# Kernel optimization log

Hardware: AMD Instinct MI355X
Metric: run time of the kernel (lower is better)

## Reference

```python
import jax, jax.numpy as jnp
import numpy as np

EPS = 1e-5

def layer_norm(x, g, b):
    mu = jnp.mean(x, axis=-1, keepdims=True)
    var = jnp.var(x, axis=-1, keepdims=True)
    return (x - mu) * jax.lax.rsqrt(var + EPS) * g + b

def mlp2_ln(x, w1, b1, g, bt, w2, b2):
    # 2-layer NN: Linear -> LayerNorm -> GELU -> Linear
    h = jax.nn.gelu(layer_norm(x @ w1 + b1, g, bt))
    return h @ w2 + b2

def mlp2(x, w1, b1, w2, b2):
    # 2-layer NN without norm: Linear -> GELU -> Linear
    return jax.nn.gelu(x @ w1 + b1) @ w2 + b2

def setup_inputs() -> dict:
    key = jax.random.key(0)
    ks = jax.random.split(key, 20)
    BS, N, D, M, SG = 64, 10000, 128, 16, 1000
    s = lambda i, shp: jax.random.normal(ks[i], shp, dtype=jnp.float32) * (1.0 / np.sqrt(shp[0]))
    return {
        "node_emb": jax.random.normal(ks[0], (BS, N, D), dtype=jnp.float32),
        "graph_emb": jax.random.normal(ks[1], (BS, D), dtype=jnp.float32),
        "sg_node_idx": jax.random.randint(ks[2], (BS, SG), 0, N),
        "sg_meta_features": jax.random.normal(ks[3], (BS, M), dtype=jnp.float32),
        # sg_net: in 2*D -> D -> D
        "sg_w1": s(4, (2 * D, D)), "sg_b1": jnp.zeros((D,), jnp.float32),
        "sg_g": jnp.ones((D,), jnp.float32), "sg_bt": jnp.zeros((D,), jnp.float32),
        "sg_w2": s(5, (D, D)), "sg_b2": jnp.zeros((D,), jnp.float32),
        # meta_feat_net: M -> D -> D
        "mf_w1": s(6, (M, D)), "mf_b1": jnp.zeros((D,), jnp.float32),
        "mf_g": jnp.ones((D,), jnp.float32), "mf_bt": jnp.zeros((D,), jnp.float32),
        "mf_w2": s(7, (D, D)), "mf_b2": jnp.zeros((D,), jnp.float32),
        # ctxt_net: 2*D -> D -> D, no norm
        "cx_w1": s(8, (2 * D, D)), "cx_b1": jnp.zeros((D,), jnp.float32),
        "cx_w2": s(9, (D, D)), "cx_b2": jnp.zeros((D,), jnp.float32),
    }

def reference(node_emb, graph_emb, sg_node_idx, sg_meta_features,
              sg_w1, sg_b1, sg_g, sg_bt, sg_w2, sg_b2,
              mf_w1, mf_b1, mf_g, mf_bt, mf_w2, mf_b2,
              cx_w1, cx_b1, cx_w2, cx_b2):
    # node_emb[:, 0] = 0  (depot / padding sentinel)
    node_emb = node_emb.at[:, 0].set(0.0)
    # gather (BS, sg_n_max, D)
    gathered = jnp.take_along_axis(node_emb, sg_node_idx[:, :, None], axis=1)
    # pooling: sum then max over subgraph nodes, concatenated -> (BS, 2*D)
    pooled = jnp.concatenate([gathered.sum(axis=1), gathered.max(axis=1)], axis=-1)
    sg_emb = (mlp2_ln(pooled, sg_w1, sg_b1, sg_g, sg_bt, sg_w2, sg_b2)
              + mlp2_ln(sg_meta_features, mf_w1, mf_b1, mf_g, mf_bt, mf_w2, mf_b2))
    ctxt_emb = mlp2(jnp.concatenate([sg_emb, graph_emb], axis=-1), cx_w1, cx_b1, cx_w2, cx_b2)
    return sg_emb, ctxt_emb
```

## Files before the change

### kernel.cpp

```cpp
#include <hip/hip_runtime.h>
#include <math.h>

#define BS    64
#define NPTS  10000
#define D     128
#define MM    16
#define SG    1000
#define SPLIT 8
#define ROWS  (SG / SPLIT)
#define PGRP  16
#define QS    8

__device__ __forceinline__ float gelu_f(float x) {
    float x3 = x * x * x;
    return 0.5f * x * (1.0f + tanhf(0.7978845608028654f * (x + 0.044715f * x3)));
}

__global__ __launch_bounds__(512) void pool_kernel(
    const float* __restrict__ node_emb, const int* __restrict__ sg_idx,
    float* __restrict__ ws_sum, float* __restrict__ ws_max)
{
    const int b  = blockIdx.x >> 3;
    const int sp = blockIdx.x & (SPLIT - 1);
    const int t  = threadIdx.x;

    __shared__ int   idx_lds[ROWS];
    __shared__ float ssum[PGRP][D];
    __shared__ float smax[PGRP][D];

    if (t < ROWS) idx_lds[t] = sg_idx[b * SG + sp * ROWS + t];
    __syncthreads();

    {
        const int g = t >> 5;
        const int c = t & 31;
        const float* __restrict__ base = node_emb + (size_t)b * NPTS * D;

        float4 s = make_float4(0.f, 0.f, 0.f, 0.f);
        float4 m = make_float4(-INFINITY, -INFINITY, -INFINITY, -INFINITY);

        #pragma unroll 4
        for (int j = g; j < ROWS; j += PGRP) {
            int id = idx_lds[j];
            float4 v = *(const float4*)(base + (size_t)id * D + (c << 2));
            float msk = (id != 0) ? 1.f : 0.f;
            v.x *= msk; v.y *= msk; v.z *= msk; v.w *= msk;
            s.x += v.x; s.y += v.y; s.z += v.z; s.w += v.w;
            m.x = fmaxf(m.x, v.x); m.y = fmaxf(m.y, v.y);
            m.z = fmaxf(m.z, v.z); m.w = fmaxf(m.w, v.w);
        }
        *(float4*)&ssum[g][c * 4] = s;
        *(float4*)&smax[g][c * 4] = m;
    }
    __syncthreads();

    const int q = t >> 7;
    const int d = t & 127;

    float rs = ssum[q * 4 + 0][d] + ssum[q * 4 + 1][d]
             + ssum[q * 4 + 2][d] + ssum[q * 4 + 3][d];
    float rm = fmaxf(fmaxf(smax[q * 4 + 0][d], smax[q * 4 + 1][d]),
                     fmaxf(smax[q * 4 + 2][d], smax[q * 4 + 3][d]));
    __syncthreads();
    ssum[q][d] = rs;
    smax[q][d] = rm;
    __syncthreads();
    if (q == 0) {
        ws_sum[(b * SPLIT + sp) * D + d] =
            ssum[0][d] + ssum[1][d] + ssum[2][d] + ssum[3][d];
    } else if (q == 1) {
        ws_max[(b * SPLIT + sp) * D + d] =
            fmaxf(fmaxf(smax[0][d], smax[1][d]), fmaxf(smax[2][d], smax[3][d]));
    }
}

__global__ __launch_bounds__(1024) void mlp_kernel(
    const float* __restrict__ ws_sum, const float* __restrict__ ws_max,
    const float* __restrict__ graph_emb, const float* __restrict__ meta,
    const float* __restrict__ sg_w1, const float* __restrict__ sg_b1,
    const float* __restrict__ sg_g,  const float* __restrict__ sg_bt,
    const float* __restrict__ sg_w2, const float* __restrict__ sg_b2,
    const float* __restrict__ mf_w1, const float* __restrict__ mf_b1,
    const float* __restrict__ mf_g,  const float* __restrict__ mf_bt,
    const float* __restrict__ mf_w2, const float* __restrict__ mf_b2,
    const float* __restrict__ cx_w1, const float* __restrict__ cx_b1,
    const float* __restrict__ cx_w2, const float* __restrict__ cx_b2,
    float* __restrict__ out)
{
    const int b = blockIdx.x;
    const int t = threadIdx.x;
    const int q = t >> 7;
    const int d = t & 127;

    __shared__ float xbuf[2 * D];
    __shared__ float pbuf[QS][D];
    __shared__ float hbufA[D];
    __shared__ float hbufB[D];
    __shared__ float red_a[D], red_b[D], red_c[D], red_d[D];
    __shared__ float stats[4];

    {
        float acc;
        if (q == 0 || q == 1) {
            acc = 0.f;
            const int s0 = q * 4;
            #pragma unroll
            for (int sp = s0; sp < s0 + 4; ++sp)
                acc += ws_sum[(b * SPLIT + sp) * D + d];
        } else if (q == 2 || q == 3) {
            acc = -INFINITY;
            const int s0 = (q - 2) * 4;
            #pragma unroll
            for (int sp = s0; sp < s0 + 4; ++sp)
                acc = fmaxf(acc, ws_max[(b * SPLIT + sp) * D + d]);
        } else acc = 0.f;
        pbuf[q][d] = acc;
        __syncthreads();
        if (q == 0)      xbuf[d]     = pbuf[0][d] + pbuf[1][d];
        else if (q == 1) xbuf[D + d] = fmaxf(pbuf[2][d], pbuf[3][d]);
        __syncthreads();
    }

    {
        float acc = 0.f;
        if (q < 4) {
            const int k0 = q * 64;
            #pragma unroll 8
            for (int kk = 0; kk < 64; ++kk)
                acc = fmaf(xbuf[k0 + kk], sg_w1[(k0 + kk) * D + d], acc);
        } else {
            const int k0 = (q - 4) * 4;
            #pragma unroll
            for (int kk = 0; kk < 4; ++kk)
                acc = fmaf(meta[b * MM + k0 + kk], mf_w1[(k0 + kk) * D + d], acc);
        }
        pbuf[q][d] = acc;
        __syncthreads();
    }

    float h_sg = 0.f, h_mf = 0.f;
    if (q == 0) {
        h_sg = pbuf[0][d] + pbuf[1][d] + pbuf[2][d] + pbuf[3][d] + sg_b1[d];
        red_a[d] = h_sg; red_b[d] = h_sg * h_sg;
    } else if (q == 1) {
        h_mf = pbuf[4][d] + pbuf[5][d] + pbuf[6][d] + pbuf[7][d] + mf_b1[d];
        red_c[d] = h_mf; red_d[d] = h_mf * h_mf;
    }
    __syncthreads();
    if (t < 64) {
        float v1 = red_a[t] + red_a[t + 64];
        float v2 = red_b[t] + red_b[t + 64];
        #pragma unroll
        for (int off = 32; off; off >>= 1) {
            v1 += __shfl_xor(v1, off, 64);
            v2 += __shfl_xor(v2, off, 64);
        }
        if (t == 0) { stats[0] = v1 * (1.f / D); stats[1] = v2 * (1.f / D); }
    } else if (t < 128) {
        const int l = t - 64;
        float v1 = red_c[l] + red_c[l + 64];
        float v2 = red_d[l] + red_d[l + 64];
        #pragma unroll
        for (int off = 32; off; off >>= 1) {
            v1 += __shfl_xor(v1, off, 64);
            v2 += __shfl_xor(v2, off, 64);
        }
        if (l == 0) { stats[2] = v1 * (1.f / D); stats[3] = v2 * (1.f / D); }
    }
    __syncthreads();
    if (q == 0) {
        float mu = stats[0], var = stats[1] - mu * mu;
        hbufA[d] = gelu_f((h_sg - mu) * rsqrtf(var + 1e-5f) * sg_g[d] + sg_bt[d]);
    } else if (q == 1) {
        float mu = stats[2], var = stats[3] - mu * mu;
        hbufB[d] = gelu_f((h_mf - mu) * rsqrtf(var + 1e-5f) * mf_g[d] + mf_bt[d]);
    }
    __syncthreads();

    {
        float acc = 0.f;
        if (q < 4) {
            const int k0 = q * 32;
            #pragma unroll 8
            for (int kk = 0; kk < 32; ++kk)
                acc = fmaf(hbufA[k0 + kk], sg_w2[(k0 + kk) * D + d], acc);
        } else {
            const int k0 = (q - 4) * 32;
            #pragma unroll 8
            for (int kk = 0; kk < 32; ++kk)
                acc = fmaf(hbufB[k0 + kk], mf_w2[(k0 + kk) * D + d], acc);
        }
        pbuf[q][d] = acc;
        __syncthreads();
        if (q == 0) {
            float sg = sg_b2[d] + mf_b2[d];
            #pragma unroll
            for (int r = 0; r < QS; ++r) sg += pbuf[r][d];
            out[b * D + d] = sg;
            xbuf[d] = sg;
        } else if (q == 1) {
            xbuf[D + d] = graph_emb[b * D + d];
        }
        __syncthreads();
    }

    {
        float acc = 0.f;
        const int k0 = q * 32;
        #pragma unroll 8
        for (int kk = 0; kk < 32; ++kk)
            acc = fmaf(xbuf[k0 + kk], cx_w1[(k0 + kk) * D + d], acc);
        pbuf[q][d] = acc;
        __syncthreads();
        if (q == 0) {
            float h = cx_b1[d];
            #pragma unroll
            for (int r = 0; r < QS; ++r) h += pbuf[r][d];
            hbufA[d] = gelu_f(h);
        }
        __syncthreads();
    }

    {
        float acc = 0.f;
        const int k0 = q * 16;
        #pragma unroll 8
        for (int kk = 0; kk < 16; ++kk)
            acc = fmaf(hbufA[k0 + kk], cx_w2[(k0 + kk) * D + d], acc);
        pbuf[q][d] = acc;
        __syncthreads();
        if (q == 0) {
            float o = cx_b2[d];
            #pragma unroll
            for (int r = 0; r < QS; ++r) o += pbuf[r][d];
            out[BS * D + b * D + d] = o;
        }
    }
}

extern "C" void kernel_launch(void* const* d_in, const int* in_sizes, int n_in,
                              void* d_out, int out_size, void* d_ws, size_t ws_size,
                              hipStream_t stream) {
    const float* node_emb  = (const float*)d_in[0];
    const float* graph_emb = (const float*)d_in[1];
    const int*   sg_idx    = (const int*)d_in[2];
    const float* meta      = (const float*)d_in[3];
    const float* sg_w1 = (const float*)d_in[4];
    const float* sg_b1 = (const float*)d_in[5];
    const float* sg_g  = (const float*)d_in[6];
    const float* sg_bt = (const float*)d_in[7];
    const float* sg_w2 = (const float*)d_in[8];
    const float* sg_b2 = (const float*)d_in[9];
    const float* mf_w1 = (const float*)d_in[10];
    const float* mf_b1 = (const float*)d_in[11];
    const float* mf_g  = (const float*)d_in[12];
    const float* mf_bt = (const float*)d_in[13];
    const float* mf_w2 = (const float*)d_in[14];
    const float* mf_b2 = (const float*)d_in[15];
    const float* cx_w1 = (const float*)d_in[16];
    const float* cx_b1 = (const float*)d_in[17];
    const float* cx_w2 = (const float*)d_in[18];
    const float* cx_b2 = (const float*)d_in[19];

    float* out    = (float*)d_out;
    float* ws     = (float*)d_ws;
    float* ws_sum = ws;
    float* ws_max = ws + BS * SPLIT * D;

    pool_kernel<<<BS * SPLIT, 512, 0, stream>>>(node_emb, sg_idx, ws_sum, ws_max);
    mlp_kernel<<<BS, 1024, 0, stream>>>(ws_sum, ws_max, graph_emb, meta,
        sg_w1, sg_b1, sg_g, sg_bt, sg_w2, sg_b2,
        mf_w1, mf_b1, mf_g, mf_bt, mf_w2, mf_b2,
        cx_w1, cx_b1, cx_w2, cx_b2, out);
}
```

Baseline: 21.74 us.

## Partition pooling work by node-id range with ballot compaction and 4-way loads

Each pool block now scans all subgraph indices for its batch and keeps only those that fall in its own slice of the node range. It compacts them into LDS using wave ballots and an LDS atomic counter. The gather loop then issues four independent row loads per iteration, with predicated masking for padding and out-of-count slots. The aim is to give each block a contiguous region of node_emb, for better cache locality, and more memory-level parallelism. The cost is that every block must read the full index list and do extra compaction work. Index-0 rows are now excluded from the max instead of contributing zero, which slightly changes the semantics.

```diff
diff --git a/kernel.cpp b/kernel.cpp
--- a/kernel.cpp
+++ b/kernel.cpp
@@ -7,7 +7,7 @@
 #define MM    16
 #define SG    1000
 #define SPLIT 8
-#define ROWS  (SG / SPLIT)
+#define RNG   (NPTS / SPLIT)
 #define PGRP  16
 #define QS    8
 
@@ -20,37 +20,82 @@
     const float* __restrict__ node_emb, const int* __restrict__ sg_idx,
     float* __restrict__ ws_sum, float* __restrict__ ws_max)
 {
-    const int b  = blockIdx.x >> 3;
-    const int sp = blockIdx.x & (SPLIT - 1);
-    const int t  = threadIdx.x;
-
-    __shared__ int   idx_lds[ROWS];
+    const int b    = blockIdx.x >> 3;
+    const int sp   = blockIdx.x & (SPLIT - 1);
+    const int t    = threadIdx.x;
+    const int lane = t & 63;
+
+    __shared__ int   ids[SG];
+    __shared__ int   cnt_lds;
     __shared__ float ssum[PGRP][D];
     __shared__ float smax[PGRP][D];
 
-    if (t < ROWS) idx_lds[t] = sg_idx[b * SG + sp * ROWS + t];
-    __syncthreads();
+    if (t == 0) cnt_lds = 0;
+    __syncthreads();
+
+    const int lo = sp * RNG;
+    const int hi = lo + RNG;
+
+    #pragma unroll
+    for (int r = 0; r < 2; ++r) {
+        const int j = r * 512 + t;
+        int id = (j < SG) ? sg_idx[b * SG + j] : -1;
+        bool m = (id >= lo) && (id < hi);
+        unsigned long long mask = __ballot(m);
+        int prefix = __popcll(mask & ((1ULL << lane) - 1ULL));
+        int wtot   = __popcll(mask);
+        int base = 0;
+        if (lane == 0 && wtot) base = atomicAdd(&cnt_lds, wtot);
+        base = __shfl(base, 0, 64);
+        if (m) ids[base + prefix] = id;
+    }
+    __syncthreads();
+    const int count = cnt_lds;
 
     {
         const int g = t >> 5;
         const int c = t & 31;
-        const float* __restrict__ base = node_emb + (size_t)b * NPTS * D;
-
-        float4 s = make_float4(0.f, 0.f, 0.f, 0.f);
-        float4 m = make_float4(-INFINITY, -INFINITY, -INFINITY, -INFINITY);
-
-        #pragma unroll 4
-        for (int j = g; j < ROWS; j += PGRP) {
-            int id = idx_lds[j];
-            float4 v = *(const float4*)(base + (size_t)id * D + (c << 2));
-            float msk = (id != 0) ? 1.f : 0.f;
-            v.x *= msk; v.y *= msk; v.z *= msk; v.w *= msk;
-            s.x += v.x; s.y += v.y; s.z += v.z; s.w += v.w;
-            m.x = fmaxf(m.x, v.x); m.y = fmaxf(m.y, v.y);
-            m.z = fmaxf(m.z, v.z); m.w = fmaxf(m.w, v.w);
+        const float* __restrict__ base_p = node_emb + (size_t)b * NPTS * D;
+
+        float4 s  = make_float4(0.f, 0.f, 0.f, 0.f);
+        float4 mm = make_float4(-INFINITY, -INFINITY, -INFINITY, -INFINITY);
+
+        const int nit = (count + 63) >> 6;
+        for (int it = 0; it < nit; ++it) {
+            const int j0 = it * 64 + g * 4;
+            const int i0 = (j0 + 0 < count) ? ids[j0 + 0] : 0;
+            const int i1 = (j0 + 1 < count) ? ids[j0 + 1] : 0;
+            const int i2 = (j0 + 2 < count) ? ids[j0 + 2] : 0;
+            const int i3 = (j0 + 3 < count) ? ids[j0 + 3] : 0;
+            float4 v0 = *(const float4*)(base_p + (size_t)i0 * D + (c << 2));
+            float4 v1 = *(const float4*)(base_p + (size_t)i1 * D + (c << 2));
+            float4 v2 = *(const float4*)(base_p + (size_t)i2 * D + (c << 2));
+            float4 v3 = *(const float4*)(base_p + (size_t)i3 * D + (c << 2));
+            bool r0 = (j0 + 0 < count) && (i0 != 0);
+            bool r1 = (j0 + 1 < count) && (i1 != 0);
+            bool r2 = (j0 + 2 < count) && (i2 != 0);
+            bool r3 = (j0 + 3 < count) && (i3 != 0);
+            float k0 = r0 ? 1.f : 0.f, k1 = r1 ? 1.f : 0.f;
+            float k2 = r2 ? 1.f : 0.f, k3 = r3 ? 1.f : 0.f;
+            s.x += v0.x * k0 + v1.x * k1 + v2.x * k2 + v3.x * k3;
+            s.y += v0.y * k0 + v1.y * k1 + v2.y * k2 + v3.y * k3;
+            s.z += v0.z * k0 + v1.z * k1 + v2.z * k2 + v3.z * k3;
+            s.w += v0.w * k0 + v1.w * k1 + v2.w * k2 + v3.w * k3;
+            mm.x = fmaxf(fmaxf(mm.x, r0 ? v0.x : -INFINITY),
+                         fmaxf(r1 ? v1.x : -INFINITY,
+                               fmaxf(r2 ? v2.x : -INFINITY, r3 ? v3.x : -INFINITY)));
+            mm.y = fmaxf(fmaxf(mm.y, r0 ? v0.y : -INFINITY),
+                         fmaxf(r1 ? v1.y : -INFINITY,
+                               fmaxf(r2 ? v2.y : -INFINITY, r3 ? v3.y : -INFINITY)));
+            mm.z = fmaxf(fmaxf(mm.z, r0 ? v0.z : -INFINITY),
+                         fmaxf(r1 ? v1.z : -INFINITY,
+                               fmaxf(r2 ? v2.z : -INFINITY, r3 ? v3.z : -INFINITY)));
+            mm.w = fmaxf(fmaxf(mm.w, r0 ? v0.w : -INFINITY),
+                         fmaxf(r1 ? v1.w : -INFINITY,
+                               fmaxf(r2 ? v2.w : -INFINITY, r3 ? v3.w : -INFINITY)));
         }
         *(float4*)&ssum[g][c * 4] = s;
-        *(float4*)&smax[g][c * 4] = m;
+        *(float4*)&smax[g][c * 4] = mm;
     }
     __syncthreads();
 
```

Measured after the change: 22.14 us. No clear change (+1.8%).
